# Kernel optimization log

Measured on AMD Instinct MI355X. Metric: run time of the kernel, lower is better.

## Reference

```python
import jax, jax.numpy as jnp
import numpy as np

VERTICES = np.array([[-1.0, -1.0, 1.0], [-1.0, 1.0, 1.0], [1.0, 1.0, 1.0], [1.0, -1.0, 1.0]], dtype=np.float32)  # [4,3]


def _gather2d(img, yi, xi):
    # img: [C,IH,IW], yi/xi: [OH,OW] int32 -> [C,OH,OW]
    return img[:, yi, xi]


def _grid_sample_bilinear_zero(inp, grid):
    # inp: [B,C,IH,IW], grid: [B,OH,OW,2] in [-1,1] (x,y), align_corners=True (old torch semantics)
    B, C, IH, IW = inp.shape
    gx = grid[..., 0]
    gy = grid[..., 1]
    ix = (gx + 1.0) * (IW - 1) * 0.5
    iy = (gy + 1.0) * (IH - 1) * 0.5
    x0 = jnp.floor(ix)
    y0 = jnp.floor(iy)
    x1 = x0 + 1.0
    y1 = y0 + 1.0
    wx1 = ix - x0  # frac weights
    wy1 = iy - y0
    wx0 = 1.0 - wx1
    wy0 = 1.0 - wy1

    def corner(xf, yf, w):
        inb = ((xf >= 0) & (xf <= IW - 1) & (yf >= 0) & (yf <= IH - 1)).astype(inp.dtype)
        xi = jnp.clip(xf, 0, IW - 1).astype(jnp.int32)
        yi = jnp.clip(yf, 0, IH - 1).astype(jnp.int32)
        vals = jax.vmap(_gather2d)(inp, yi, xi)  # [B,C,OH,OW]
        return vals * (w * inb)[:, None, :, :]

    out = (corner(x0, y0, wx0 * wy0) + corner(x1, y0, wx1 * wy0)
           + corner(x0, y1, wx0 * wy1) + corner(x1, y1, wx1 * wy1))
    return out


def affine_spatial_transform(inp, theta, OH, OW):
    B, C, IH, IW = inp.shape
    hs = jnp.linspace(-1.0, 1.0, OH)
    ws = jnp.linspace(-1.0, 1.0, OW)
    hh = jnp.broadcast_to(hs[:, None], (OH, OW))
    ww = jnp.broadcast_to(ws[None, :], (OH, OW))
    t = jnp.stack([ww, hh, jnp.ones((OH, OW), dtype=inp.dtype)], axis=2)  # [OH,OW,3]
    # source_grid = theta @ t : [B,OH,OW,2]
    grid = jnp.einsum('bij,hwj->bhwi', theta, t)
    out = _grid_sample_bilinear_zero(inp, grid)
    v = jnp.asarray(VERTICES)  # [4,3]
    vout = jnp.einsum('bij,vj->bvi', theta, v)  # [B,4,2]
    x_coord = (vout[..., 0] + 1.0) * IW * 0.5
    y_coord = (vout[..., 1] + 1.0) * IH * 0.5
    vertices_out = jnp.stack([x_coord, y_coord], axis=2)  # [B,4,2]
    return out, vertices_out


def setup_inputs() -> dict:
    key = jax.random.key(0)
    k1, k2 = jax.random.split(key)
    B, C, IH, IW = 16, 64, 256, 256
    inp = jax.random.normal(k1, (B, C, IH, IW), dtype=jnp.float32)
    theta = jax.random.normal(k2, (B, 2, 3), dtype=jnp.float32)
    return {"input": inp, "theta": theta, "OH": 256, "OW": 256}


def reference(input, theta, OH, OW):
    return affine_spatial_transform(input, theta, OH, OW)
```

## Files before the change

kernel.cpp:

```cpp
#include <hip/hip_runtime.h>

#define B  16
#define C  64
#define IH 256
#define IW 256
#define OH 256
#define OW 256

#define TW 16
#define TH 16
#define NWT (OW / TW)
#define NHT (OH / TH)
#define NB  (B * NHT * NWT)
#define CAPU 2048
#define CAPF (CAPU + 256)

typedef float f4 __attribute__((ext_vector_type(4)));
typedef float f2 __attribute__((ext_vector_type(2)));
typedef f2 __attribute__((aligned(4))) f2u;

#define BAR() do {                                         \
    asm volatile("s_waitcnt lgkmcnt(0)" ::: "memory");     \
    __builtin_amdgcn_s_barrier();                          \
    asm volatile("" ::: "memory");                         \
} while (0)

__global__ __launch_bounds__(256, 8) void ast_fused(const float* __restrict__ inp,
                                                    const float* __restrict__ theta,
                                                    float* __restrict__ out) {
    const int tid = threadIdx.x;

    if (blockIdx.x == 0 && tid < B * 4) {
        const int b_ = tid >> 2;
        const int v  = tid & 3;
        const float vx_tab[4] = {-1.0f, -1.0f, 1.0f, 1.0f};
        const float vy_tab[4] = {-1.0f,  1.0f, 1.0f, -1.0f};
        const float Vx = vx_tab[v];
        const float Vy = vy_tab[v];
        const float ox = theta[b_*6+0]*Vx + theta[b_*6+1]*Vy + theta[b_*6+2];
        const float oy = theta[b_*6+3]*Vx + theta[b_*6+4]*Vy + theta[b_*6+5];
        float* vo = out + (size_t)B * C * OH * OW;
        vo[b_*8 + v*2 + 0] = (ox + 1.0f) * ((float)IW * 0.5f);
        vo[b_*8 + v*2 + 1] = (oy + 1.0f) * ((float)IH * 0.5f);
    }

    int id = (int)blockIdx.x;
    id = (id & 7) * (NB >> 3) + (id >> 3);

    const int wt = id & (NWT - 1);
    const int ht = (id >> 4) & (NHT - 1);
    const int b  = id >> 8;

    const int tx = tid & (TW - 1);
    const int ty = tid >> 4;
    const int w = wt * TW + tx;
    const int h = ht * TH + ty;

    const float t00 = theta[b*6+0], t01 = theta[b*6+1], t02 = theta[b*6+2];
    const float t10 = theta[b*6+3], t11 = theta[b*6+4], t12 = theta[b*6+5];

    const float sWn = 2.0f / (float)(OW - 1);
    const float sHn = 2.0f / (float)(OH - 1);

    const float wn = -1.0f + sWn * (float)w;
    const float hn = -1.0f + sHn * (float)h;
    const float ix = (t00 * wn + t01 * hn + t02 + 1.0f) * ((float)(IW - 1) * 0.5f);
    const float iy = (t10 * wn + t11 * hn + t12 + 1.0f) * ((float)(IH - 1) * 0.5f);

    const float x0f = floorf(ix);
    const float y0f = floorf(iy);
    const float wx1 = ix - x0f;
    const float wy1 = iy - y0f;
    const float wx0 = 1.0f - wx1;
    const float wy0 = 1.0f - wy1;

    const bool inx0 = (x0f >= 0.0f) && (x0f <= (float)(IW - 1));
    const bool inx1 = (x0f + 1.0f >= 0.0f) && (x0f + 1.0f <= (float)(IW - 1));
    const bool iny0 = (y0f >= 0.0f) && (y0f <= (float)(IH - 1));
    const bool iny1 = (y0f + 1.0f >= 0.0f) && (y0f + 1.0f <= (float)(IH - 1));

    const float w00 = (inx0 && iny0) ? wx0 * wy0 : 0.0f;
    const float w10 = (inx1 && iny0) ? wx1 * wy0 : 0.0f;
    const float w01 = (inx0 && iny1) ? wx0 * wy1 : 0.0f;
    const float w11 = (inx1 && iny1) ? wx1 * wy1 : 0.0f;

    const float wnA = -1.0f + sWn * (float)(wt * TW);
    const float wnB = -1.0f + sWn * (float)(wt * TW + TW - 1);
    const float hnA = -1.0f + sHn * (float)(ht * TH);
    const float hnB = -1.0f + sHn * (float)(ht * TH + TH - 1);

    const float ixAA = (t00*wnA + t01*hnA + t02 + 1.0f) * 127.5f;
    const float ixAB = (t00*wnA + t01*hnB + t02 + 1.0f) * 127.5f;
    const float ixBA = (t00*wnB + t01*hnA + t02 + 1.0f) * 127.5f;
    const float ixBB = (t00*wnB + t01*hnB + t02 + 1.0f) * 127.5f;
    const float iyAA = (t10*wnA + t11*hnA + t12 + 1.0f) * 127.5f;
    const float iyAB = (t10*wnA + t11*hnB + t12 + 1.0f) * 127.5f;
    const float iyBA = (t10*wnB + t11*hnA + t12 + 1.0f) * 127.5f;
    const float iyBB = (t10*wnB + t11*hnB + t12 + 1.0f) * 127.5f;

    const float min_ix = fminf(fminf(ixAA, ixAB), fminf(ixBA, ixBB));
    const float max_ix = fmaxf(fmaxf(ixAA, ixAB), fmaxf(ixBA, ixBB));
    const float min_iy = fminf(fminf(iyAA, iyAB), fminf(iyBA, iyBB));
    const float max_iy = fmaxf(fmaxf(iyAA, iyAB), fmaxf(iyBA, iyBB));

    float* o = out + ((size_t)(b * C) << 16) + (size_t)(h * OW + w);

    if (max_ix < -1.0f || min_ix > 256.0f || max_iy < -1.0f || min_iy > 256.0f) {
        #pragma unroll 8
        for (int c = 0; c < C; ++c) {
            __builtin_nontemporal_store(0.0f, o);
            o += OH * OW;
        }
        return;
    }

    const int bx0 = min(max((int)floorf(min_ix) - 1, 0), IW - 1);
    const int bx1 = min(max((int)floorf(max_ix) + 2, 0), IW - 1);
    const int by0 = min(max((int)floorf(min_iy) - 1, 0), IH - 1);
    const int by1 = min(max((int)floorf(max_iy) + 2, 0), IH - 1);

    const int Wneed = bx1 - bx0 + 4;
    int lw = 32 - __builtin_clz((unsigned)(Wneed - 1));
    if (lw < 3) lw = 3;
    if (lw > 8) lw = 8;
    const int P    = 1 << lw;
    const int Pp   = P + 4;
    const int ax0p = min(bx0 & ~3, IW - P);
    const int Hd   = by1 - by0 + 1;

    const int x0i = (int)x0f;
    const int y0i = (int)y0f;
    const float* plane = inp + ((size_t)(b * C) << 16);

    if (Hd * Pp > CAPU) {
        const int  basex = min(max(x0i, 0), IW - 2);
        const bool sA = (x0i <= IW - 2);
        const bool sB = (x0i >= 0);
        const int  y0c = min(max(y0i,     0), IH - 1);
        const int  y1c = min(max(y0i + 1, 0), IH - 1);
        const int off0 = y0c * IW + basex;
        const int off1 = y1c * IW + basex;
        const float* pl = plane;
        for (int c = 0; c < C; ++c) {
            const f2 ra = *(const f2u*)(pl + off0);
            const f2 rb = *(const f2u*)(pl + off1);
            const float a00 = sA ? ra.x : ra.y;
            const float a10 = sB ? ra.y : ra.x;
            const float b00 = sA ? rb.x : rb.y;
            const float b11 = sB ? rb.y : rb.x;
            float v = w00 * a00;
            v = fmaf(w10, a10, v);
            v = fmaf(w01, b00, v);
            v = fmaf(w11, b11, v);
            __builtin_nontemporal_store(v, o);
            pl += IH * IW;
            o  += OH * OW;
        }
        return;
    }

    const int xin = x0i - ax0p;
    const int rin = y0i - by0;
    const int xc0 = min(max(xin, 0), P - 2);
    const bool selA = (xin <= P - 2);
    const bool selB = (xin >= 0);
    const int r0 = min(max(rin,     0), Hd - 1);
    const int r1 = min(max(rin + 1, 0), Hd - 1);
    const int ad0 = r0 * Pp + xc0;
    const int ad1 = r1 * Pp + xc0;

    const int S = Hd << lw;
    int gsrc[2], ldst[2];
    #pragma unroll
    for (int g = 0; g < 2; ++g) {
        const int i4 = g * 1024 + (tid << 2);
        if (i4 < S) {
            const int r  = i4 >> lw;
            const int xb = i4 & (P - 1);
            gsrc[g] = (by0 + r) * IW + ax0p + xb;
            ldst[g] = r * Pp + xb;
        } else {
            gsrc[g] = by0 * IW + ax0p;
            ldst[g] = CAPU + ((tid & 63) << 2);
        }
    }

    __shared__ float sb[2][CAPF];
    float* const b0 = &sb[0][0];
    float* const b1 = &sb[1][0];

    auto samp = [&](const float* Lb) -> float {
        const float p00 = Lb[ad0], p01 = Lb[ad0 + 1];
        const float p10 = Lb[ad1], p11 = Lb[ad1 + 1];
        const float a00 = selA ? p00 : p01;
        const float a10 = selB ? p01 : p00;
        const float c00 = selA ? p10 : p11;
        const float c11 = selB ? p11 : p10;
        float v = w00 * a00;
        v = fmaf(w10, a10, v);
        v = fmaf(w01, c00, v);
        v = fmaf(w11, c11, v);
        return v;
    };

    const float* pld = plane;
    f4 pfA0, pfA1, pfB0, pfB1;

    pfA0 = *(const f4*)(pld + gsrc[0]);
    pfA1 = *(const f4*)(pld + gsrc[1]);
    pld += IH * IW;
    pfB0 = *(const f4*)(pld + gsrc[0]);
    pfB1 = *(const f4*)(pld + gsrc[1]);
    pld += IH * IW;
    *(f4*)(b0 + ldst[0]) = pfA0;
    *(f4*)(b0 + ldst[1]) = pfA1;
    BAR();

    #pragma unroll 1
    for (int k = 0; k < 31; ++k) {
        pfA0 = *(const f4*)(pld + gsrc[0]);
        pfA1 = *(const f4*)(pld + gsrc[1]);
        pld += IH * IW;
        *(f4*)(b1 + ldst[0]) = pfB0;
        *(f4*)(b1 + ldst[1]) = pfB1;
        const float v0 = samp(b0);
        BAR();
        __builtin_nontemporal_store(v0, o);
        o += OH * OW;

        pfB0 = *(const f4*)(pld + gsrc[0]);
        pfB1 = *(const f4*)(pld + gsrc[1]);
        pld += IH * IW;
        *(f4*)(b0 + ldst[0]) = pfA0;
        *(f4*)(b0 + ldst[1]) = pfA1;
        const float v1 = samp(b1);
        BAR();
        __builtin_nontemporal_store(v1, o);
        o += OH * OW;
    }

    *(f4*)(b1 + ldst[0]) = pfB0;
    *(f4*)(b1 + ldst[1]) = pfB1;
    const float v62 = samp(b0);
    BAR();
    __builtin_nontemporal_store(v62, o);
    o += OH * OW;
    const float v63 = samp(b1);
    __builtin_nontemporal_store(v63, o);
}

extern "C" void kernel_launch(void* const* d_in, const int* in_sizes, int n_in,
                              void* d_out, int out_size, void* d_ws, size_t ws_size,
                              hipStream_t stream) {
    const float* inp   = (const float*)d_in[0];
    const float* theta = (const float*)d_in[1];
    float* out = (float*)d_out;

    ast_fused<<<NB, 256, 0, stream>>>(inp, theta, out);
}
```

Baseline: 529.5 us.

## Process two channels per pipeline stage to halve barriers and deepen prefetch

The channel loop now stages two channel planes per buffer instead of one, so each barrier covers two samples and twice as many global loads are in flight. The staging capacity per plane shrinks from 2048 to 1280 floats, and the occupancy hint drops from 8 to 6 blocks per SM to make room for the extra registers. The smaller capacity risks overflowing for footprints that the old 2048 limit handled, unless the hidden fallback path covers that case, and occupancy may drop.

```diff
diff --git a/kernel.cpp b/kernel.cpp
--- a/kernel.cpp
+++ b/kernel.cpp
@@ -12,8 +12,8 @@
 #define NWT (OW / TW)
 #define NHT (OH / TH)
 #define NB  (B * NHT * NWT)
-#define CAPU 2048
-#define CAPF (CAPU + 256)
+#define CAPU 1280
+#define CAPF 1536
 
 typedef float f4 __attribute__((ext_vector_type(4)));
 typedef float f2 __attribute__((ext_vector_type(2)));
@@ -25,7 +25,7 @@
     asm volatile("" ::: "memory");                         \
 } while (0)
 
-__global__ __launch_bounds__(256, 8) void ast_fused(const float* __restrict__ inp,
+__global__ __launch_bounds__(256, 6) void ast_fused(const float* __restrict__ inp,
                                                     const float* __restrict__ theta,
                                                     float* __restrict__ out) {
     const int tid = threadIdx.x;
@@ -185,9 +185,7 @@
         }
     }
 
-    __shared__ float sb[2][CAPF];
-    float* const b0 = &sb[0][0];
-    float* const b1 = &sb[1][0];
+    __shared__ float sb[2][2][CAPF];
 
     auto samp = [&](const float* Lb) -> float {
         const float p00 = Lb[ad0], p01 = Lb[ad0 + 1];
@@ -203,50 +201,73 @@
         return v;
     };
 
+    const size_t PL = (size_t)(IH * IW);
     const float* pld = plane;
-    f4 pfA0, pfA1, pfB0, pfB1;
-
-    pfA0 = *(const f4*)(pld + gsrc[0]);
-    pfA1 = *(const f4*)(pld + gsrc[1]);
-    pld += IH * IW;
-    pfB0 = *(const f4*)(pld + gsrc[0]);
-    pfB1 = *(const f4*)(pld + gsrc[1]);
-    pld += IH * IW;
-    *(f4*)(b0 + ldst[0]) = pfA0;
-    *(f4*)(b0 + ldst[1]) = pfA1;
+    f4 pfA00, pfA01, pfA10, pfA11;
+    f4 pfB00, pfB01, pfB10, pfB11;
+
+    pfA00 = *(const f4*)(pld + gsrc[0]);
+    pfA01 = *(const f4*)(pld + gsrc[1]);
+    pfA10 = *(const f4*)(pld + PL + gsrc[0]);
+    pfA11 = *(const f4*)(pld + PL + gsrc[1]);
+    pld += 2 * PL;
+    pfB00 = *(const f4*)(pld + gsrc[0]);
+    pfB01 = *(const f4*)(pld + gsrc[1]);
+    pfB10 = *(const f4*)(pld + PL + gsrc[0]);
+    pfB11 = *(const f4*)(pld + PL + gsrc[1]);
+    pld += 2 * PL;
+    *(f4*)(&sb[0][0][0] + ldst[0]) = pfA00;
+    *(f4*)(&sb[0][0][0] + ldst[1]) = pfA01;
+    *(f4*)(&sb[0][1][0] + ldst[0]) = pfA10;
+    *(f4*)(&sb[0][1][0] + ldst[1]) = pfA11;
     BAR();
 
     #pragma unroll 1
-    for (int k = 0; k < 31; ++k) {
-        pfA0 = *(const f4*)(pld + gsrc[0]);
-        pfA1 = *(const f4*)(pld + gsrc[1]);
-        pld += IH * IW;
-        *(f4*)(b1 + ldst[0]) = pfB0;
-        *(f4*)(b1 + ldst[1]) = pfB1;
-        const float v0 = samp(b0);
+    for (int k = 0; k < 15; ++k) {
+        pfA00 = *(const f4*)(pld + gsrc[0]);
+        pfA01 = *(const f4*)(pld + gsrc[1]);
+        pfA10 = *(const f4*)(pld + PL + gsrc[0]);
+        pfA11 = *(const f4*)(pld + PL + gsrc[1]);
+        pld += 2 * PL;
+        *(f4*)(&sb[1][0][0] + ldst[0]) = pfB00;
+        *(f4*)(&sb[1][0][0] + ldst[1]) = pfB01;
+        *(f4*)(&sb[1][1][0] + ldst[0]) = pfB10;
+        *(f4*)(&sb[1][1][0] + ldst[1]) = pfB11;
+        const float v0 = samp(&sb[0][0][0]);
+        const float v1 = samp(&sb[0][1][0]);
         BAR();
-        __builtin_nontemporal_store(v0, o);
-        o += OH * OW;
-
-        pfB0 = *(const f4*)(pld + gsrc[0]);
-        pfB1 = *(const f4*)(pld + gsrc[1]);
-        pld += IH * IW;
-        *(f4*)(b0 + ldst[0]) = pfA0;
-        *(f4*)(b0 + ldst[1]) = pfA1;
-        const float v1 = samp(b1);
+        __builtin_nontemporal_store(v0, o);  o += OH * OW;
+        __builtin_nontemporal_store(v1, o);  o += OH * OW;
+
+        pfB00 = *(const f4*)(pld + gsrc[0]);
+        pfB01 = *(const f4*)(pld + gsrc[1]);
+        pfB10 = *(const f4*)(pld + PL + gsrc[0]);
+        pfB11 = *(const f4*)(pld + PL + gsrc[1]);
+        pld += 2 * PL;
+        *(f4*)(&sb[0][0][0] + ldst[0]) = pfA00;
+        *(f4*)(&sb[0][0][0] + ldst[1]) = pfA01;
+        *(f4*)(&sb[0][1][0] + ldst[0]) = pfA10;
+        *(f4*)(&sb[0][1][0] + ldst[1]) = pfA11;
+        const float v2 = samp(&sb[1][0][0]);
+        const float v3 = samp(&sb[1][1][0]);
         BAR();
-        __builtin_nontemporal_store(v1, o);
-        o += OH * OW;
-    }
-
-    *(f4*)(b1 + ldst[0]) = pfB0;
-    *(f4*)(b1 + ldst[1]) = pfB1;
-    const float v62 = samp(b0);
+        __builtin_nontemporal_store(v2, o);  o += OH * OW;
+        __builtin_nontemporal_store(v3, o);  o += OH * OW;
+    }
+
+    *(f4*)(&sb[1][0][0] + ldst[0]) = pfB00;
+    *(f4*)(&sb[1][0][0] + ldst[1]) = pfB01;
+    *(f4*)(&sb[1][1][0] + ldst[0]) = pfB10;
+    *(f4*)(&sb[1][1][0] + ldst[1]) = pfB11;
+    const float v0 = samp(&sb[0][0][0]);
+    const float v1 = samp(&sb[0][1][0]);
     BAR();
-    __builtin_nontemporal_store(v62, o);
-    o += OH * OW;
-    const float v63 = samp(b1);
-    __builtin_nontemporal_store(v63, o);
+    __builtin_nontemporal_store(v0, o);  o += OH * OW;
+    __builtin_nontemporal_store(v1, o);  o += OH * OW;
+    const float v2 = samp(&sb[1][0][0]);
+    const float v3 = samp(&sb[1][1][0]);
+    __builtin_nontemporal_store(v2, o);  o += OH * OW;
+    __builtin_nontemporal_store(v3, o);
 }
 
 extern "C" void kernel_launch(void* const* d_in, const int* in_sizes, int n_in,
```

Result: no change. 527.8 us (-0.3%).
